# Kernel optimization log

Hardware: AMD Instinct MI355X
Metric: run time of the kernel (lower is better)

Reference implementation:

```python
import jax, jax.numpy as jnp
import numpy as np

REF_GROUND_RES = 0.2  # reference_ground_resolution
PR_MIN = 0.2          # pr_min


def setup_inputs() -> dict:
    key = jax.random.key(0)
    k1, k2, k3, k4 = jax.random.split(key, 4)
    B, H, W, N = 8, 512, 512, 128
    pred_hm = jax.random.normal(k1, (B, 1, H, W), dtype=jnp.float32)
    pred_sm = jax.random.normal(k2, (B, 1, H, W), dtype=jnp.float32)
    # per-sample ground resolution in [0.1, 0.5] (avoid divide-by-zero)
    ground_resolution = jax.random.uniform(k3, (B,), dtype=jnp.float32) * 0.4 + 0.1
    mask = jnp.ones((B, 1, H, W), dtype=jnp.float32)
    centers = jax.random.randint(k4, (B, N, 2), 0, H, dtype=jnp.int32)
    return {"pred_hm": pred_hm, "pred_sm": pred_sm,
            "ground_resolution": ground_resolution, "mask": mask,
            "centers": centers}


def _draw_gaussian_broadcast(H, W, centers_f, sigmas):
    # centers_f: [N,2] float (row, col); sigmas: [N]
    yy = jnp.arange(H, dtype=centers_f.dtype)
    xx = jnp.arange(W, dtype=centers_f.dtype)
    dy2 = (yy[None, :] - centers_f[:, 0:1]) ** 2            # [N,H]
    dx2 = (xx[None, :] - centers_f[:, 1:2]) ** 2            # [N,W]
    d2 = dy2[:, :, None] + dx2[:, None, :]                   # [N,H,W]
    g = jnp.exp(-d2 / (2.0 * (sigmas[:, None, None] ** 2)))  # per-center gaussian
    return jnp.max(g, axis=0)                                 # [H,W] max-splat


def reference(pred_hm, pred_sm, ground_resolution, mask, centers):
    B, _, H, W = pred_hm.shape

    def per_sample(hm, sm, c, gr, m):
        sm0 = sm[0]                                # [H,W]
        scale_loss = jnp.mean(sm0 ** 2)
        c = jnp.clip(c, 0, H - 1)                   # clamp like torch.clamp(..., max=H-1)
        # predicted per-center sigma from scale map at the center locations
        sizes = PR_MIN / gr + jax.nn.relu(sm0[c[:, 0], c[:, 1]]) * REF_GROUND_RES / gr
        gt = _draw_gaussian_broadcast(H, W, c.astype(hm.dtype), sizes)
        hm_loss = jnp.mean((hm[0] - gt) ** 2 * m[0])
        return scale_loss, hm_loss, gt

    sl, hl, gts = jax.vmap(per_sample)(pred_hm, pred_sm, centers,
                                       ground_resolution, mask)
    return jnp.mean(sl), jnp.mean(hl), gts[:, None, :, :]
```

## Files before the change

### kernel.cpp

```cpp
#include <hip/hip_runtime.h>

#define HH 512
#define WW 512
#define NB 8
#define NC 128
#define TW 64
#define TH 16
#define NTILES 256
#define NBLK (NB * NTILES)
#define CUT 30.0f


__global__ __launch_bounds__(256) void ahl_main_kernel(
    const float* __restrict__ pred_hm,
    const float* __restrict__ pred_sm,
    const float* __restrict__ mask,
    const float* __restrict__ ground_res,
    const int*   __restrict__ centers,
    float* __restrict__ out,
    float2* __restrict__ partials) {
    __shared__ float4 sp[NC];
    __shared__ float4 sc[NC];
    __shared__ int s_cnt;
    __shared__ float red[8];

    const int b    = blockIdx.x >> 8;
    const int tile = blockIdx.x & 255;
    const int tx0  = (tile & 7) * TW;
    const int ty0  = (tile >> 3) * TH;
    const int tid  = threadIdx.x;

    const int cg  = tid & 15;
    const int row = tid >> 4;
    const int x0  = tx0 + cg * 4;
    const int y   = ty0 + row;

    const size_t sbase = (size_t)b * HH * WW;
    const size_t idx   = sbase + (size_t)y * WW + x0;
    float4 hm4 = *(const float4*)&pred_hm[idx];
    float4 sm4 = *(const float4*)&pred_sm[idx];
    float4 mk4 = *(const float4*)&mask[idx];

    if (tid == 0) s_cnt = 0;
    if (tid < NC) {
        int cy = centers[(b * NC + tid) * 2 + 0];
        int cx = centers[(b * NC + tid) * 2 + 1];
        cy = min(max(cy, 0), HH - 1);
        cx = min(max(cx, 0), WW - 1);
        float smv = pred_sm[sbase + (size_t)cy * WW + cx];
        float g   = ground_res[b];
        float size = (0.2f / g) * (1.0f + fmaxf(smv, 0.0f));
        float s = 0.70710678f / size;
        sp[tid] = make_float4(s, -(float)cx * s, -(float)cy * s, 0.0f);
    }
    __syncthreads();

    if (tid < NC) {
        float4 P = sp[tid];
        float a0 = fmaf((float)tx0,            P.x, P.y);
        float a1 = fmaf((float)(tx0 + TW - 1), P.x, P.y);
        float b0 = fmaf((float)ty0,            P.x, P.z);
        float b1 = fmaf((float)(ty0 + TH - 1), P.x, P.z);
        float dx = fmaxf(0.0f, fmaxf(a0, -a1));
        float dy = fmaxf(0.0f, fmaxf(b0, -b1));
        if (fmaf(dx, dx, dy * dy) < CUT) {
            int i = atomicAdd(&s_cnt, 1);
            sc[i] = P;
        }
    }
    __syncthreads();
    const int cnt = s_cnt;

    const float yfv = (float)y;
    float xf[4];
#pragma unroll
    for (int j = 0; j < 4; j++) xf[j] = (float)(x0 + j);
    float m[4] = {1e30f, 1e30f, 1e30f, 1e30f};

    for (int i = 0; i < cnt; i++) {
        float4 P = sc[i];
        float dys = fmaf(yfv, P.x, P.z);
        float a = dys * dys;
#pragma unroll
        for (int j = 0; j < 4; j++) {
            float d = fmaf(xf[j], P.x, P.y);
            m[j] = fminf(m[j], fmaf(d, d, a));
        }
    }

    float g0 = __expf(-m[0]);
    float g1 = __expf(-m[1]);
    float g2 = __expf(-m[2]);
    float g3 = __expf(-m[3]);
    float2* gp = (float2*)&out[2 + idx];
    gp[0] = make_float2(g0, g1);
    gp[1] = make_float2(g2, g3);

    float d0 = hm4.x - g0, d1 = hm4.y - g1, d2 = hm4.z - g2, d3 = hm4.w - g3;
    float lhm = d0 * d0 * mk4.x;
    lhm = fmaf(d1 * d1, mk4.y, lhm);
    lhm = fmaf(d2 * d2, mk4.z, lhm);
    lhm = fmaf(d3 * d3, mk4.w, lhm);
    float lsc = sm4.x * sm4.x;
    lsc = fmaf(sm4.y, sm4.y, lsc);
    lsc = fmaf(sm4.z, sm4.z, lsc);
    lsc = fmaf(sm4.w, sm4.w, lsc);

#pragma unroll
    for (int off = 32; off > 0; off >>= 1) {
        lhm += __shfl_down(lhm, off);
        lsc += __shfl_down(lsc, off);
    }
    int lane = tid & 63, wid = tid >> 6;
    if (lane == 0) { red[wid] = lsc; red[4 + wid] = lhm; }
    __syncthreads();
    if (tid == 0) {
        float ts = red[0] + red[1] + red[2] + red[3];
        float th = red[4] + red[5] + red[6] + red[7];
        partials[blockIdx.x] = make_float2(ts, th);
    }
}

__global__ __launch_bounds__(256) void ahl_reduce_kernel(
    const float2* __restrict__ partials, float* __restrict__ out) {
    __shared__ float red[8];
    const int tid = threadIdx.x;
    float ts = 0.0f, th = 0.0f;
    for (int s = tid; s < NBLK; s += 256) {
        float2 a = partials[s];
        ts += a.x;
        th += a.y;
    }
#pragma unroll
    for (int off = 32; off > 0; off >>= 1) {
        ts += __shfl_down(ts, off);
        th += __shfl_down(th, off);
    }
    int lane = tid & 63, wid = tid >> 6;
    if (lane == 0) { red[wid] = ts; red[4 + wid] = th; }
    __syncthreads();
    if (tid == 0) {
        const float invc = 1.0f / (float)((size_t)NB * HH * WW);
        out[0] = (red[0] + red[1] + red[2] + red[3]) * invc;
        out[1] = (red[4] + red[5] + red[6] + red[7]) * invc;
    }
}

extern "C" void kernel_launch(void* const* d_in, const int* in_sizes, int n_in,
                              void* d_out, int out_size, void* d_ws, size_t ws_size,
                              hipStream_t stream) {
    const float* pred_hm    = (const float*)d_in[0];
    const float* pred_sm    = (const float*)d_in[1];
    const float* ground_res = (const float*)d_in[2];
    const float* mask       = (const float*)d_in[3];
    const int*   centers    = (const int*)d_in[4];
    float* out = (float*)d_out;
    float2* partials = (float2*)d_ws;

    ahl_main_kernel<<<NBLK, 256, 0, stream>>>(pred_hm, pred_sm, mask,
                                              ground_res, centers, out,
                                              partials);
    ahl_reduce_kernel<<<1, 256, 0, stream>>>(partials, out);
}
```

Measured before the change: 86.59 us.

## Enlarge tiles to 64x64 with two rows per thread and 512-thread blocks

Changes the per-block tile from 64x16 to 64x64 and launches 512 threads per block, each computing two rows 32 apart so the x-distance term per center is shared between the two rows. This amortizes per-block center setup and culling over four times more pixels and cuts the block count. In exchange the coarser tile passes more centers through the culling test, increasing inner-loop work per pixel, and the smaller grid may reduce latency hiding.

```diff
diff --git a/kernel.cpp b/kernel.cpp
--- a/kernel.cpp
+++ b/kernel.cpp
@@ -4,14 +4,13 @@
 #define WW 512
 #define NB 8
 #define NC 128
-#define TW 64
-#define TH 16
-#define NTILES 256
+#define TS 64
+#define NTILES 64
 #define NBLK (NB * NTILES)
 #define CUT 30.0f
 
 
-__global__ __launch_bounds__(256) void ahl_main_kernel(
+__global__ __launch_bounds__(512) void ahl_main_kernel(
     const float* __restrict__ pred_hm,
     const float* __restrict__ pred_sm,
     const float* __restrict__ mask,
@@ -22,24 +21,30 @@
     __shared__ float4 sp[NC];
     __shared__ float4 sc[NC];
     __shared__ int s_cnt;
-    __shared__ float red[8];
+    __shared__ float redS[8];
+    __shared__ float redH[8];
 
-    const int b    = blockIdx.x >> 8;
-    const int tile = blockIdx.x & 255;
-    const int tx0  = (tile & 7) * TW;
-    const int ty0  = (tile >> 3) * TH;
+    const int b    = blockIdx.x >> 6;
+    const int tile = blockIdx.x & 63;
+    const int tx0  = (tile & 7) * TS;
+    const int ty0  = (tile >> 3) * TS;
     const int tid  = threadIdx.x;
 
     const int cg  = tid & 15;
-    const int row = tid >> 4;
+    const int r0  = tid >> 4;
     const int x0  = tx0 + cg * 4;
-    const int y   = ty0 + row;
+    const int ya  = ty0 + r0;
+    const int yb  = ya + 32;
 
-    const size_t sbase = (size_t)b * HH * WW;
-    const size_t idx   = sbase + (size_t)y * WW + x0;
-    float4 hm4 = *(const float4*)&pred_hm[idx];
-    float4 sm4 = *(const float4*)&pred_sm[idx];
-    float4 mk4 = *(const float4*)&mask[idx];
+    const size_t sbase = (size_t)b * (HH * WW);
+    const size_t ia    = sbase + (size_t)ya * WW + x0;
+    const size_t ib    = sbase + (size_t)yb * WW + x0;
+    float4 hmA = *(const float4*)&pred_hm[ia];
+    float4 smA = *(const float4*)&pred_sm[ia];
+    float4 mkA = *(const float4*)&mask[ia];
+    float4 hmB = *(const float4*)&pred_hm[ib];
+    float4 smB = *(const float4*)&pred_sm[ib];
+    float4 mkB = *(const float4*)&mask[ib];
 
     if (tid == 0) s_cnt = 0;
     if (tid < NC) {
@@ -58,9 +63,9 @@
     if (tid < NC) {
         float4 P = sp[tid];
         float a0 = fmaf((float)tx0,            P.x, P.y);
-        float a1 = fmaf((float)(tx0 + TW - 1), P.x, P.y);
+        float a1 = fmaf((float)(tx0 + TS - 1), P.x, P.y);
         float b0 = fmaf((float)ty0,            P.x, P.z);
-        float b1 = fmaf((float)(ty0 + TH - 1), P.x, P.z);
+        float b1 = fmaf((float)(ty0 + TS - 1), P.x, P.z);
         float dx = fmaxf(0.0f, fmaxf(a0, -a1));
         float dy = fmaxf(0.0f, fmaxf(b0, -b1));
         if (fmaf(dx, dx, dy * dy) < CUT) {
@@ -71,40 +76,58 @@
     __syncthreads();
     const int cnt = s_cnt;
 
-    const float yfv = (float)y;
+    const float yfa = (float)ya;
+    const float yfb = (float)yb;
     float xf[4];
 #pragma unroll
     for (int j = 0; j < 4; j++) xf[j] = (float)(x0 + j);
-    float m[4] = {1e30f, 1e30f, 1e30f, 1e30f};
+    float mA[4] = {1e30f, 1e30f, 1e30f, 1e30f};
+    float mB[4] = {1e30f, 1e30f, 1e30f, 1e30f};
 
     for (int i = 0; i < cnt; i++) {
         float4 P = sc[i];
-        float dys = fmaf(yfv, P.x, P.z);
-        float a = dys * dys;
+        float da = fmaf(yfa, P.x, P.z); da *= da;
+        float db = fmaf(yfb, P.x, P.z); db *= db;
 #pragma unroll
         for (int j = 0; j < 4; j++) {
-            float d = fmaf(xf[j], P.x, P.y);
-            m[j] = fminf(m[j], fmaf(d, d, a));
+            float d  = fmaf(xf[j], P.x, P.y);
+            float dd = d * d;
+            mA[j] = fminf(mA[j], dd + da);
+            mB[j] = fminf(mB[j], dd + db);
         }
     }
 
-    float g0 = __expf(-m[0]);
-    float g1 = __expf(-m[1]);
-    float g2 = __expf(-m[2]);
-    float g3 = __expf(-m[3]);
-    float2* gp = (float2*)&out[2 + idx];
-    gp[0] = make_float2(g0, g1);
-    gp[1] = make_float2(g2, g3);
+    float gA0 = __expf(-mA[0]), gA1 = __expf(-mA[1]);
+    float gA2 = __expf(-mA[2]), gA3 = __expf(-mA[3]);
+    float gB0 = __expf(-mB[0]), gB1 = __expf(-mB[1]);
+    float gB2 = __expf(-mB[2]), gB3 = __expf(-mB[3]);
 
-    float d0 = hm4.x - g0, d1 = hm4.y - g1, d2 = hm4.z - g2, d3 = hm4.w - g3;
-    float lhm = d0 * d0 * mk4.x;
-    lhm = fmaf(d1 * d1, mk4.y, lhm);
-    lhm = fmaf(d2 * d2, mk4.z, lhm);
-    lhm = fmaf(d3 * d3, mk4.w, lhm);
-    float lsc = sm4.x * sm4.x;
-    lsc = fmaf(sm4.y, sm4.y, lsc);
-    lsc = fmaf(sm4.z, sm4.z, lsc);
-    lsc = fmaf(sm4.w, sm4.w, lsc);
+    float2* gpA = (float2*)&out[2 + ia];
+    gpA[0] = make_float2(gA0, gA1);
+    gpA[1] = make_float2(gA2, gA3);
+    float2* gpB = (float2*)&out[2 + ib];
+    gpB[0] = make_float2(gB0, gB1);
+    gpB[1] = make_float2(gB2, gB3);
+
+    float d0 = hmA.x - gA0, d1 = hmA.y - gA1, d2 = hmA.z - gA2, d3 = hmA.w - gA3;
+    float lhm = d0 * d0 * mkA.x;
+    lhm = fmaf(d1 * d1, mkA.y, lhm);
+    lhm = fmaf(d2 * d2, mkA.z, lhm);
+    lhm = fmaf(d3 * d3, mkA.w, lhm);
+    d0 = hmB.x - gB0; d1 = hmB.y - gB1; d2 = hmB.z - gB2; d3 = hmB.w - gB3;
+    lhm = fmaf(d0 * d0, mkB.x, lhm);
+    lhm = fmaf(d1 * d1, mkB.y, lhm);
+    lhm = fmaf(d2 * d2, mkB.z, lhm);
+    lhm = fmaf(d3 * d3, mkB.w, lhm);
+
+    float lsc = smA.x * smA.x;
+    lsc = fmaf(smA.y, smA.y, lsc);
+    lsc = fmaf(smA.z, smA.z, lsc);
+    lsc = fmaf(smA.w, smA.w, lsc);
+    lsc = fmaf(smB.x, smB.x, lsc);
+    lsc = fmaf(smB.y, smB.y, lsc);
+    lsc = fmaf(smB.z, smB.z, lsc);
+    lsc = fmaf(smB.w, smB.w, lsc);
 
 #pragma unroll
     for (int off = 32; off > 0; off >>= 1) {
@@ -112,11 +135,12 @@
         lsc += __shfl_down(lsc, off);
     }
     int lane = tid & 63, wid = tid >> 6;
-    if (lane == 0) { red[wid] = lsc; red[4 + wid] = lhm; }
+    if (lane == 0) { redS[wid] = lsc; redH[wid] = lhm; }
     __syncthreads();
     if (tid == 0) {
-        float ts = red[0] + red[1] + red[2] + red[3];
-        float th = red[4] + red[5] + red[6] + red[7];
+        float ts = 0.0f, th = 0.0f;
+#pragma unroll
+        for (int w = 0; w < 8; w++) { ts += redS[w]; th += redH[w]; }
         partials[blockIdx.x] = make_float2(ts, th);
     }
 }
@@ -157,7 +181,7 @@
     float* out = (float*)d_out;
     float2* partials = (float2*)d_ws;
 
-    ahl_main_kernel<<<NBLK, 256, 0, stream>>>(pred_hm, pred_sm, mask,
+    ahl_main_kernel<<<NBLK, 512, 0, stream>>>(pred_hm, pred_sm, mask,
                                               ground_res, centers, out,
                                               partials);
     ahl_reduce_kernel<<<1, 256, 0, stream>>>(partials, out);
```

After: 83.92 us. -3.1%, faster.
